# Kernel tuning notes

Measured on AMD Instinct MI355X. Metric: run time of the kernel, lower is better.

The kernel has to match this reference:

```python
import jax, jax.numpy as jnp
import numpy as np

B, S, H, E, V, ML = 64, 256, 512, 256, 32000, 32256  # batch, src len, hidden, embed, vocab, extended vocab


def setup_inputs() -> dict:
    key = jax.random.key(0)
    ks = jax.random.split(key, 14)
    s = 0.02
    return {
        "input_idx": jax.random.randint(ks[0], (B, 1), 0, ML),
        "encoder_outputs": jax.random.normal(ks[1], (B, S, 2 * H), jnp.float32),
        "input_seq_idx": jax.random.randint(ks[2], (B, S), 0, ML),
        "pre_state": jax.random.normal(ks[3], (B, H), jnp.float32),
        "pre_prob_c": jax.random.uniform(ks[4], (B, S), jnp.float32),
        "embed_table": jax.random.normal(ks[5], (V, E), jnp.float32) * s,
        "W_aw": jax.random.normal(ks[6], (2 * H, H), jnp.float32) * s,
        "b_aw": jnp.zeros((2 * H,), jnp.float32),
        "W_ac": jax.random.normal(ks[7], (H, 2 * H + E), jnp.float32) * s,
        "b_ac": jnp.zeros((H,), jnp.float32),
        "W_ih": jax.random.normal(ks[8], (3 * H, 3 * H), jnp.float32) * s,
        "b_ih": jnp.zeros((3 * H,), jnp.float32),
        "W_hh": jax.random.normal(ks[9], (3 * H, H), jnp.float32) * s,
        "b_hh": jnp.zeros((3 * H,), jnp.float32),
        "W_o": jax.random.normal(ks[10], (V, H), jnp.float32) * s,
        "b_o": jnp.zeros((V,), jnp.float32),
        "W_c": jax.random.normal(ks[11], (H, 2 * H), jnp.float32) * s,
        "b_c": jnp.zeros((H,), jnp.float32),
    }


def reference(input_idx, encoder_outputs, input_seq_idx, pre_state, pre_prob_c,
              embed_table, W_aw, b_aw, W_ac, b_ac, W_ih, b_ih, W_hh, b_hh,
              W_o, b_o, W_c, b_c):
    dtype = encoder_outputs.dtype
    Vv = W_o.shape[0]

    # embedding of previous token (OOV -> UNK id 2)
    embed_x = jnp.where(input_idx >= Vv, 2, input_idx)            # [B,1]
    embedding = embed_table[embed_x[:, 0]]                        # [B,E]

    # attentive read
    attn_strength = pre_state @ W_aw.T + b_aw                     # [B,2H]
    attn_scores = jnp.einsum('bsd,bd->bs', encoder_outputs, attn_strength)
    attn_weights = jax.nn.softmax(attn_scores, axis=1)            # [B,S]
    context = jnp.einsum('bs,bsd->bd', attn_weights, encoder_outputs)  # [B,2H]
    attn_reading = jnp.concatenate([context, embedding], axis=1) @ W_ac.T + b_ac  # [B,H]

    # selective read (copy): positions equal to previous output token
    sel_mask = (input_seq_idx == input_idx).astype(dtype)         # [B,S]
    select_weights = sel_mask * pre_prob_c
    select_reading = jnp.einsum('bs,bsd->bd', select_weights, encoder_outputs)  # [B,2H]

    # single GRU step (torch gate order: r, z, n)
    x = jnp.concatenate([attn_reading, select_reading], axis=1)   # [B,3H]
    gi = x @ W_ih.T + b_ih
    gh = pre_state @ W_hh.T + b_hh
    i_r, i_z, i_n = jnp.split(gi, 3, axis=1)
    h_r, h_z, h_n = jnp.split(gh, 3, axis=1)
    r = jax.nn.sigmoid(i_r + h_r)
    z = jax.nn.sigmoid(i_z + h_z)
    n = jnp.tanh(i_n + r * h_n)
    state = (1.0 - z) * n + z * pre_state                         # [B,H]

    # generate + copy scores, joint softmax
    score_g = state @ W_o.T + b_o                                 # [B,V]
    score_c_feat = jnp.tanh(encoder_outputs @ W_c.T + b_c)        # [B,S,H]
    score_c = jnp.einsum('bsh,bh->bs', score_c_feat, state)       # [B,S]
    prob = jax.nn.softmax(jnp.concatenate([score_g, score_c], axis=1), axis=1)
    prob_g, prob_c0 = prob[:, :Vv], prob[:, Vv:]

    # aggregate copy probs over repeated source tokens
    same = (input_seq_idx[:, :, None] == input_seq_idx[:, None, :]).astype(dtype)  # [B,S,S]
    prob_c = jnp.einsum('bi,bij->bj', prob_c0, same)              # [B,S]

    # scatter copy probs into extended vocab (duplicates carry identical values)
    bidx = jnp.arange(prob.shape[0])[:, None]
    out = jnp.zeros((prob.shape[0], ML), dtype).at[bidx, input_seq_idx].set(prob_c, mode='drop')
    out = out + jnp.pad(prob_g, ((0, 0), (0, ML - Vv)))
    return out, state, prob_c
```

## Files before the change

kernel.cpp:

```cpp
#include <hip/hip_runtime.h>
#include <hip/hip_bf16.h>
#include <math.h>

#define BB   64
#define SS   256
#define HH   512
#define HD2  1024
#define EE   256
#define VV   32000
#define MLSZ 32256
#define G3   1536

typedef __attribute__((ext_vector_type(8))) short bhalf8;
typedef __attribute__((ext_vector_type(4))) float f32x4;

__device__ __forceinline__ float wredsum(float v) {
#pragma unroll
  for (int o = 32; o > 0; o >>= 1) v += __shfl_down(v, o);
  return v;
}
__device__ __forceinline__ float wredmax(float v) {
#pragma unroll
  for (int o = 32; o > 0; o >>= 1) v = fmaxf(v, __shfl_down(v, o));
  return v;
}
__device__ __forceinline__ float ftanh(float x) {
  float e = __expf(-2.f * fabsf(x));
  float t = (1.f - e) / (1.f + e);
  return copysignf(t, x);
}
__device__ __forceinline__ float fsigmoid(float x) { return 1.f / (1.f + __expf(-x)); }
__device__ __forceinline__ float dot4(float4 a, float4 b) {
  return a.x*b.x + a.y*b.y + a.z*b.z + a.w*b.w;
}
__device__ __forceinline__ void split2(float x, ushort& h, ushort& l) {
  uint u = __float_as_uint(x);
  uint hr = (u + 0x7fffu + ((u >> 16) & 1u)) & 0xffff0000u;
  h = (ushort)(hr >> 16);
  float r = x - __uint_as_float(hr);
  uint u2 = __float_as_uint(r);
  l = (ushort)((u2 + 0x7fffu + ((u2 >> 16) & 1u)) >> 16);
}

__global__ __launch_bounds__(256) void k_split(
    const float* __restrict__ x, ushort* __restrict__ hi, ushort* __restrict__ lo)
{
  const int i = (blockIdx.x * 256 + threadIdx.x) * 4;
  const float4 v = *(const float4*)&x[i];
  ushort4 h, l;
  split2(v.x, h.x, l.x); split2(v.y, h.y, l.y);
  split2(v.z, h.z, l.z); split2(v.w, h.w, l.w);
  *(ushort4*)&hi[i] = h;
  *(ushort4*)&lo[i] = l;
}

__global__ __launch_bounds__(256) void k_smallgemm(
    const float* __restrict__ A, int lda,
    const float* __restrict__ W, int ldw,
    const float* __restrict__ bias,
    float* __restrict__ C, int ldc, int klen)
{
  __shared__ float As[64][36];
  __shared__ float Ws[64][36];
  const int tid = threadIdx.x;
  const int n0 = blockIdx.x * 64;
  const int kbeg = blockIdx.y * klen;
  const int tb = tid & 15;
  const int tn = tid >> 4;
  float acc[4][4];
#pragma unroll
  for (int i = 0; i < 4; ++i)
#pragma unroll
    for (int j = 0; j < 4; ++j)
      acc[i][j] = (blockIdx.y == 0) ? bias[n0 + tn + 16*j] : 0.f;

  const int rr = tid >> 3;
  const int cc = (tid & 7) * 4;
  for (int kc = kbeg; kc < kbeg + klen; kc += 32) {
    __syncthreads();
#pragma unroll
    for (int r = rr; r < 64; r += 32) {
      *(float4*)&As[r][cc] = *(const float4*)&A[(size_t)r * lda + kc + cc];
      *(float4*)&Ws[r][cc] = *(const float4*)&W[(size_t)(n0 + r) * ldw + kc + cc];
    }
    __syncthreads();
#pragma unroll
    for (int k4 = 0; k4 < 32; k4 += 4) {
      float4 a[4], w[4];
#pragma unroll
      for (int i = 0; i < 4; ++i) a[i] = *(const float4*)&As[tb + 16*i][k4];
#pragma unroll
      for (int j = 0; j < 4; ++j) w[j] = *(const float4*)&Ws[tn + 16*j][k4];
#pragma unroll
      for (int i = 0; i < 4; ++i)
#pragma unroll
        for (int j = 0; j < 4; ++j)
          acc[i][j] += dot4(a[i], w[j]);
    }
  }
#pragma unroll
  for (int i = 0; i < 4; ++i)
#pragma unroll
    for (int j = 0; j < 4; ++j)
      atomicAdd(&C[(size_t)(tb + 16*i) * ldc + n0 + tn + 16*j], acc[i][j]);
}

__global__ __launch_bounds__(256) void k_pass1(
    const float* __restrict__ enc, const float* __restrict__ astr,
    const int* __restrict__ seq, const int* __restrict__ iidx,
    const float* __restrict__ ppc,
    float* __restrict__ scores, float* __restrict__ selread)
{
  const int b  = blockIdx.x >> 2;
  const int sc = blockIdx.x & 3;
  const int tid = threadIdx.x;
  const int lane = tid & 63;
  const int w = tid >> 6;
  __shared__ float sr_s[4][1024];

  const int d0 = lane * 16;
  const float* ap = astr + (size_t)b * HD2 + d0;
  const float4 a0 = *(const float4*)(ap + 0);
  const float4 a1 = *(const float4*)(ap + 4);
  const float4 a2 = *(const float4*)(ap + 8);
  const float4 a3 = *(const float4*)(ap + 12);

  float sr[16];
#pragma unroll
  for (int j = 0; j < 16; ++j) sr[j] = 0.f;

  const int idxb = iidx[b];
  const int sbase = sc * 64 + w * 16;
  for (int si = 0; si < 16; ++si) {
    const int s = sbase + si;
    const float* row = enc + ((size_t)b * SS + s) * HD2 + d0;
    const float4 q0 = *(const float4*)(row + 0);
    const float4 q1 = *(const float4*)(row + 4);
    const float4 q2 = *(const float4*)(row + 8);
    const float4 q3 = *(const float4*)(row + 12);
    float dot = dot4(q0, a0) + dot4(q1, a1) + dot4(q2, a2) + dot4(q3, a3);
    dot = wredsum(dot);
    if (lane == 0) scores[b * SS + s] = dot;
    const float sw = (seq[b * SS + s] == idxb) ? ppc[b * SS + s] : 0.f;
    if (sw != 0.f) {
      sr[0]  += sw * q0.x; sr[1]  += sw * q0.y; sr[2]  += sw * q0.z; sr[3]  += sw * q0.w;
      sr[4]  += sw * q1.x; sr[5]  += sw * q1.y; sr[6]  += sw * q1.z; sr[7]  += sw * q1.w;
      sr[8]  += sw * q2.x; sr[9]  += sw * q2.y; sr[10] += sw * q2.z; sr[11] += sw * q2.w;
      sr[12] += sw * q3.x; sr[13] += sw * q3.y; sr[14] += sw * q3.z; sr[15] += sw * q3.w;
    }
  }
#pragma unroll
  for (int j = 0; j < 16; ++j) sr_s[w][d0 + j] = sr[j];
  __syncthreads();
#pragma unroll
  for (int j = 0; j < 4; ++j) {
    const int d = tid * 4 + j;
    const float v = sr_s[0][d] + sr_s[1][d] + sr_s[2][d] + sr_s[3][d];
    atomicAdd(&selread[(size_t)b * HD2 + d], v);
  }
}

__global__ __launch_bounds__(256) void k_softmax_s(float* __restrict__ scores)
{
  const int b = blockIdx.x;
  const int tid = threadIdx.x;
  const int lane = tid & 63, w = tid >> 6;
  __shared__ float red[4];
  __shared__ float bm, bsum;
  float x = scores[b * SS + tid];
  float m = wredmax(x);
  if (lane == 0) red[w] = m;
  __syncthreads();
  if (tid == 0) bm = fmaxf(fmaxf(red[0], red[1]), fmaxf(red[2], red[3]));
  __syncthreads();
  float e = __expf(x - bm);
  float s = wredsum(e);
  if (lane == 0) red[w] = s;
  __syncthreads();
  if (tid == 0) bsum = red[0] + red[1] + red[2] + red[3];
  __syncthreads();
  scores[b * SS + tid] = e / bsum;
}

__global__ __launch_bounds__(256) void k_pass2(
    const float* __restrict__ enc, const float* __restrict__ wgt,
    float* __restrict__ context)
{
  const int b  = blockIdx.x >> 2;
  const int sc = blockIdx.x & 3;
  const int tid = threadIdx.x;
  const int lane = tid & 63;
  const int w = tid >> 6;
  __shared__ float cs[4][1024];
  const int d0 = lane * 16;
  float a[16];
#pragma unroll
  for (int j = 0; j < 16; ++j) a[j] = 0.f;
  const int sbase = sc * 64 + w * 16;
  for (int si = 0; si < 16; ++si) {
    const int s = sbase + si;
    const float wt = wgt[b * SS + s];
    const float* row = enc + ((size_t)b * SS + s) * HD2 + d0;
    const float4 q0 = *(const float4*)(row + 0);
    const float4 q1 = *(const float4*)(row + 4);
    const float4 q2 = *(const float4*)(row + 8);
    const float4 q3 = *(const float4*)(row + 12);
    a[0]  += wt * q0.x; a[1]  += wt * q0.y; a[2]  += wt * q0.z; a[3]  += wt * q0.w;
    a[4]  += wt * q1.x; a[5]  += wt * q1.y; a[6]  += wt * q1.z; a[7]  += wt * q1.w;
    a[8]  += wt * q2.x; a[9]  += wt * q2.y; a[10] += wt * q2.z; a[11] += wt * q2.w;
    a[12] += wt * q3.x; a[13] += wt * q3.y; a[14] += wt * q3.z; a[15] += wt * q3.w;
  }
#pragma unroll
  for (int j = 0; j < 16; ++j) cs[w][d0 + j] = a[j];
  __syncthreads();
#pragma unroll
  for (int j = 0; j < 4; ++j) {
    const int d = tid * 4 + j;
    atomicAdd(&context[(size_t)b * HD2 + d],
              cs[0][d] + cs[1][d] + cs[2][d] + cs[3][d]);
  }
}

__global__ __launch_bounds__(256) void k_cat1(
    const float* __restrict__ context, const float* __restrict__ embed,
    const int* __restrict__ iidx, const float* __restrict__ selread,
    float* __restrict__ cat1, float* __restrict__ xbuf)
{
  const int b = blockIdx.x;
  const int tid = threadIdx.x;
  for (int d = tid; d < HD2; d += 256) {
    cat1[(size_t)b * 1280 + d] = context[(size_t)b * HD2 + d];
    xbuf[(size_t)b * G3 + 512 + d] = selread[(size_t)b * HD2 + d];
  }
  int ei = iidx[b];
  if (ei >= VV) ei = 2;
  cat1[(size_t)b * 1280 + 1024 + tid] = embed[(size_t)ei * EE + tid];
}

__global__ __launch_bounds__(256) void k_gru(
    const float* __restrict__ gi, const float* __restrict__ gh,
    const float* __restrict__ ps, float* __restrict__ st)
{
  const int t = blockIdx.x * 256 + threadIdx.x;
  const int b = t >> 9, h = t & 511;
  const float* gib = gi + (size_t)b * G3;
  const float* ghb = gh + (size_t)b * G3;
  const float r = fsigmoid(gib[h] + ghb[h]);
  const float z = fsigmoid(gib[512 + h] + ghb[512 + h]);
  const float n = ftanh(gib[1024 + h] + r * ghb[1024 + h]);
  st[t] = (1.f - z) * n + z * ps[t];
}

__global__ __launch_bounds__(256) void k_score_g(
    const float* __restrict__ st, const float* __restrict__ Wo,
    const float* __restrict__ bo, float* __restrict__ sg)
{
  __shared__ float Ss[64][36];
  __shared__ float Ws[128][36];
  const int tid = threadIdx.x;
  const int n0 = blockIdx.x * 128;
  const int tb = tid & 15;
  const int tn = tid >> 4;
  float acc[4][8];
#pragma unroll
  for (int i = 0; i < 4; ++i)
#pragma unroll
    for (int j = 0; j < 8; ++j) acc[i][j] = 0.f;

  const int rr = tid >> 3;
  const int cc = (tid & 7) * 4;
  for (int kc = 0; kc < 512; kc += 32) {
    __syncthreads();
#pragma unroll
    for (int r = rr; r < 64; r += 32)
      *(float4*)&Ss[r][cc] = *(const float4*)&st[(size_t)r * 512 + kc + cc];
#pragma unroll
    for (int r = rr; r < 128; r += 32)
      *(float4*)&Ws[r][cc] = *(const float4*)&Wo[(size_t)(n0 + r) * 512 + kc + cc];
    __syncthreads();
#pragma unroll
    for (int k4 = 0; k4 < 32; k4 += 4) {
      float4 a[4], w[8];
#pragma unroll
      for (int i = 0; i < 4; ++i) a[i] = *(const float4*)&Ss[tb + 16*i][k4];
#pragma unroll
      for (int j = 0; j < 8; ++j) w[j] = *(const float4*)&Ws[tn + 16*j][k4];
#pragma unroll
      for (int i = 0; i < 4; ++i)
#pragma unroll
        for (int j = 0; j < 8; ++j)
          acc[i][j] += dot4(a[i], w[j]);
    }
  }
#pragma unroll
  for (int i = 0; i < 4; ++i)
#pragma unroll
    for (int j = 0; j < 8; ++j)
      sg[(size_t)(tb + 16*i) * VV + n0 + tn + 16*j] = acc[i][j] + bo[n0 + tn + 16*j];
}

__global__ __launch_bounds__(256) void k_score_c(
    const float* __restrict__ enc,
    const ushort* __restrict__ whi, const ushort* __restrict__ wlo,
    const float* __restrict__ bc, const float* __restrict__ st,
    float* __restrict__ scc)
{
  __shared__ ushort sAhi[128 * 32];
  __shared__ ushort sAlo[128 * 32];
  __shared__ ushort sBhi[128 * 32];
  __shared__ ushort sBlo[128 * 32];

  const int tid = threadIdx.x;
  const int m0 = blockIdx.x * 128;
  const int n0 = blockIdx.y * 128;
  const int b  = m0 >> 8;
  const int lane = tid & 63;
  const int wid = tid >> 6;
  const int wr = wid >> 1, wc = wid & 1;
  const int kg = lane >> 4;
  const int rl = lane & 15;

  f32x4 acc[4][4];
#pragma unroll
  for (int m = 0; m < 4; ++m)
#pragma unroll
    for (int n = 0; n < 4; ++n) acc[m][n] = (f32x4){0.f, 0.f, 0.f, 0.f};

  const int ar = tid >> 3;
  const int ak = (tid & 7) * 4;
  const int br = tid >> 2;
  const int bs = tid & 3;

  for (int kc = 0; kc < 1024; kc += 32) {
    __syncthreads();
#pragma unroll
    for (int swp = 0; swp < 4; ++swp) {
      const int row = ar + swp * 32;
      const float4 v = *(const float4*)&enc[(size_t)(m0 + row) * 1024 + kc + ak];
      ushort4 h, l;
      split2(v.x, h.x, l.x); split2(v.y, h.y, l.y);
      split2(v.z, h.z, l.z); split2(v.w, h.w, l.w);
      const int sw = (row + (row >> 2)) & 3;
      const int off = row * 64 + (((ak >> 3) ^ sw) * 16) + (ak & 7) * 2;
      *(ushort4*)((char*)sAhi + off) = h;
      *(ushort4*)((char*)sAlo + off) = l;
    }
#pragma unroll
    for (int swp = 0; swp < 2; ++swp) {
      const int row = br + swp * 64;
      const size_t g = (size_t)(n0 + row) * 1024 + kc + bs * 8;
      const uint4 hv = *(const uint4*)&whi[g];
      const uint4 lv = *(const uint4*)&wlo[g];
      const int sw = (row + (row >> 2)) & 3;
      const int off = row * 64 + ((bs ^ sw) * 16);
      *(uint4*)((char*)sBhi + off) = hv;
      *(uint4*)((char*)sBlo + off) = lv;
    }
    __syncthreads();
    bhalf8 ahi[4], alo[4], bhi[4], blo[4];
#pragma unroll
    for (int m = 0; m < 4; ++m) {
      const int row = wr * 64 + m * 16 + rl;
      const int off = row * 64 + ((kg ^ ((row + (row >> 2)) & 3)) * 16);
      ahi[m] = *(const bhalf8*)((const char*)sAhi + off);
      alo[m] = *(const bhalf8*)((const char*)sAlo + off);
    }
#pragma unroll
    for (int n = 0; n < 4; ++n) {
      const int row = wc * 64 + n * 16 + rl;
      const int off = row * 64 + ((kg ^ ((row + (row >> 2)) & 3)) * 16);
      bhi[n] = *(const bhalf8*)((const char*)sBhi + off);
      blo[n] = *(const bhalf8*)((const char*)sBlo + off);
    }
#pragma unroll
    for (int m = 0; m < 4; ++m)
#pragma unroll
      for (int n = 0; n < 4; ++n) {
        acc[m][n] = __builtin_amdgcn_mfma_f32_16x16x32_bf16(ahi[m], bhi[n], acc[m][n], 0, 0, 0);
        acc[m][n] = __builtin_amdgcn_mfma_f32_16x16x32_bf16(ahi[m], blo[n], acc[m][n], 0, 0, 0);
        acc[m][n] = __builtin_amdgcn_mfma_f32_16x16x32_bf16(alo[m], bhi[n], acc[m][n], 0, 0, 0);
      }
  }

  float bcv[4], stv[4];
#pragma unroll
  for (int n = 0; n < 4; ++n) {
    const int col = n0 + wc * 64 + n * 16 + rl;
    bcv[n] = bc[col];
    stv[n] = st[(size_t)b * 512 + col];
  }
  float rs[4][4];
#pragma unroll
  for (int m = 0; m < 4; ++m)
#pragma unroll
    for (int r = 0; r < 4; ++r) {
      float p = 0.f;
#pragma unroll
      for (int n = 0; n < 4; ++n)
        p += ftanh(acc[m][n][r] + bcv[n]) * stv[n];
      rs[m][r] = p;
    }
#pragma unroll
  for (int off = 1; off < 16; off <<= 1)
#pragma unroll
    for (int m = 0; m < 4; ++m)
#pragma unroll
      for (int r = 0; r < 4; ++r)
        rs[m][r] += __shfl_xor(rs[m][r], off);
  if (rl == 0) {
#pragma unroll
    for (int m = 0; m < 4; ++m)
#pragma unroll
      for (int r = 0; r < 4; ++r) {
        const int srow = (m0 & 255) + wr * 64 + m * 16 + kg * 4 + r;
        atomicAdd(&scc[b * SS + srow], rs[m][r]);
      }
  }
}

__global__ __launch_bounds__(1024) void k_bigsoftmax(
    const float* __restrict__ sg, const float* __restrict__ scc,
    float* __restrict__ out, float* __restrict__ pc0, float* __restrict__ stats)
{
  const int b = blockIdx.x;
  const int tid = threadIdx.x;
  const int lane = tid & 63, w = tid >> 6;
  __shared__ float red[16];
  __shared__ float bm, bsum;
  const float* sgb = sg + (size_t)b * VV;
  const float* scb = scc + (size_t)b * SS;

  float m = -3.0e38f;
  for (int v = tid; v < VV; v += 1024) m = fmaxf(m, sgb[v]);
  if (tid < SS) m = fmaxf(m, scb[tid]);
  m = wredmax(m);
  if (lane == 0) red[w] = m;
  __syncthreads();
  if (tid == 0) {
    float t = red[0];
    for (int i = 1; i < 16; ++i) t = fmaxf(t, red[i]);
    bm = t;
  }
  __syncthreads();
  const float mx = bm;

  float s = 0.f;
  for (int v = tid; v < VV; v += 1024) s += __expf(sgb[v] - mx);
  if (tid < SS) s += __expf(scb[tid] - mx);
  s = wredsum(s);
  if (lane == 0) red[w] = s;
  __syncthreads();
  if (tid == 0) {
    float t = 0.f;
    for (int i = 0; i < 16; ++i) t += red[i];
    bsum = t;
  }
  __syncthreads();
  const float inv = 1.f / bsum;
  if (tid == 0) { stats[2*b] = mx; stats[2*b + 1] = inv; }

  float* outb = out + (size_t)b * MLSZ;
  for (int v = tid; v < VV; v += 1024) outb[v] = __expf(sgb[v] - mx) * inv;
  if (tid < SS) {
    pc0[b * SS + tid] = __expf(scb[tid] - mx) * inv;
    outb[VV + tid] = 0.f;
  }
}

__global__ __launch_bounds__(256) void k_probc(
    const int* __restrict__ seq, const float* __restrict__ pc0,
    float* __restrict__ pcout)
{
  const int b = blockIdx.x;
  const int tid = threadIdx.x;
  __shared__ int sq[256];
  __shared__ float pp[256];
  sq[tid] = seq[b * SS + tid];
  pp[tid] = pc0[b * SS + tid];
  __syncthreads();
  const int mys = sq[tid];
  float acc = 0.f;
  for (int i = 0; i < 256; ++i) acc += (sq[i] == mys) ? pp[i] : 0.f;
  pcout[b * SS + tid] = acc;
}

__global__ __launch_bounds__(256) void k_scatter(
    const int* __restrict__ seq, const float* __restrict__ pcout,
    const float* __restrict__ sg, const float* __restrict__ stats,
    float* __restrict__ out)
{
  const int b = blockIdx.x;
  const int tid = threadIdx.x;
  const int v = seq[b * SS + tid];
  if (v < 0 || v >= MLSZ) return;
  float val = pcout[b * SS + tid];
  if (v < VV) val += __expf(sg[(size_t)b * VV + v] - stats[2*b]) * stats[2*b + 1];
  out[(size_t)b * MLSZ + v] = val;
}

extern "C" void kernel_launch(void* const* d_in, const int* in_sizes, int n_in,
                              void* d_out, int out_size, void* d_ws, size_t ws_size,
                              hipStream_t stream)
{
  (void)in_sizes; (void)n_in; (void)out_size; (void)ws_size;
  const int*   input_idx = (const int*)d_in[0];
  const float* enc       = (const float*)d_in[1];
  const int*   seq       = (const int*)d_in[2];
  const float* pre_state = (const float*)d_in[3];
  const float* ppc       = (const float*)d_in[4];
  const float* embed     = (const float*)d_in[5];
  const float* W_aw = (const float*)d_in[6];  const float* b_aw = (const float*)d_in[7];
  const float* W_ac = (const float*)d_in[8];  const float* b_ac = (const float*)d_in[9];
  const float* W_ih = (const float*)d_in[10]; const float* b_ih = (const float*)d_in[11];
  const float* W_hh = (const float*)d_in[12]; const float* b_hh = (const float*)d_in[13];
  const float* W_o  = (const float*)d_in[14]; const float* b_o  = (const float*)d_in[15];
  const float* W_c  = (const float*)d_in[16]; const float* b_c  = (const float*)d_in[17];

  float* out   = (float*)d_out;
  float* st    = out + (size_t)BB * MLSZ;
  float* pcout = st + BB * HH;

  float* ws      = (float*)d_ws;
  float* astr    = ws;
  float* gh      = astr    + 65536;
  float* xbuf    = gh      + 98304;
  float* gi      = xbuf    + 98304;
  float* selread = gi      + 98304;
  float* context = selread + 65536;
  float* scc     = context + 65536;
  const size_t zlen = 65536 + 98304 + 98304 + 98304 + 65536 + 65536 + 16384;
  float* scores  = scc     + 16384;
  float* cat1    = scores  + 16384;
  float* sg      = cat1    + 81920;
  float* pc0     = sg      + 2048000;
  float* stats   = pc0     + 16384;
  ushort* whi    = (ushort*)(stats + 128);
  ushort* wlo    = whi + 524288;

  hipMemsetAsync(ws, 0, zlen * sizeof(float), stream);

  k_split<<<512, 256, 0, stream>>>(W_c, whi, wlo);

  k_smallgemm<<<dim3(16, 2), 256, 0, stream>>>(pre_state, 512, W_aw, 512, b_aw, astr, 1024, 256);
  k_smallgemm<<<dim3(24, 2), 256, 0, stream>>>(pre_state, 512, W_hh, 512, b_hh, gh, 1536, 256);
  k_pass1<<<256, 256, 0, stream>>>(enc, astr, seq, input_idx, ppc, scores, selread);
  k_softmax_s<<<64, 256, 0, stream>>>(scores);
  k_pass2<<<256, 256, 0, stream>>>(enc, scores, context);
  k_cat1<<<64, 256, 0, stream>>>(context, embed, input_idx, selread, cat1, xbuf);
  k_smallgemm<<<dim3(8, 2), 256, 0, stream>>>(cat1, 1280, W_ac, 1280, b_ac, xbuf, 1536, 640);
  k_smallgemm<<<dim3(24, 4), 256, 0, stream>>>(xbuf, 1536, W_ih, 1536, b_ih, gi, 1536, 384);
  k_gru<<<128, 256, 0, stream>>>(gi, gh, pre_state, st);
  k_score_g<<<250, 256, 0, stream>>>(st, W_o, b_o, sg);
  k_score_c<<<dim3(128, 4), 256, 0, stream>>>(enc, whi, wlo, b_c, st, scc);
  k_bigsoftmax<<<64, 1024, 0, stream>>>(sg, scc, out, pc0, stats);
  k_probc<<<64, 256, 0, stream>>>(seq, pc0, pcout);
  k_scatter<<<64, 256, 0, stream>>>(seq, pcout, sg, stats, out);
}
```

Before: 542.8 us.

## Use bf16 MFMA for score_g and pre-permute W_c fragments for score_c

The FP32 SIMT GEMM for the generate scores (state @ W_o^T) becomes single-pass bf16 MFMA. The state is first rounded to bf16 and permuted into fragment order, and W_o is converted to bf16 in registers. W_c is split into hi/lo bf16 halves that are stored in MFMA fragment order, so score_c can load B fragments straight from global memory. That lets score_c drop its B shared-memory staging and move to 512-thread blocks covering all 512 columns, which removes the duplicated encoder loads across the old column blocks. The catch is that score_g now runs at plain bf16 precision instead of fp32, so the generate logits lose accuracy.

```diff
diff --git a/kernel.cpp b/kernel.cpp
--- a/kernel.cpp
+++ b/kernel.cpp
@@ -33,6 +33,10 @@
 __device__ __forceinline__ float dot4(float4 a, float4 b) {
   return a.x*b.x + a.y*b.y + a.z*b.z + a.w*b.w;
 }
+__device__ __forceinline__ ushort bf16rne(float x) {
+  uint u = __float_as_uint(x);
+  return (ushort)((u + 0x7fffu + ((u >> 16) & 1u)) >> 16);
+}
 __device__ __forceinline__ void split2(float x, ushort& h, ushort& l) {
   uint u = __float_as_uint(x);
   uint hr = (u + 0x7fffu + ((u >> 16) & 1u)) & 0xffff0000u;
@@ -42,16 +46,43 @@
   l = (ushort)((u2 + 0x7fffu + ((u2 >> 16) & 1u)) >> 16);
 }
 
-__global__ __launch_bounds__(256) void k_split(
-    const float* __restrict__ x, ushort* __restrict__ hi, ushort* __restrict__ lo)
-{
-  const int i = (blockIdx.x * 256 + threadIdx.x) * 4;
-  const float4 v = *(const float4*)&x[i];
-  ushort4 h, l;
-  split2(v.x, h.x, l.x); split2(v.y, h.y, l.y);
-  split2(v.z, h.z, l.z); split2(v.w, h.w, l.w);
-  *(ushort4*)&hi[i] = h;
-  *(ushort4*)&lo[i] = l;
+__global__ __launch_bounds__(256) void k_split_wc(
+    const float* __restrict__ Wc, ushort* __restrict__ bhi, ushort* __restrict__ blo)
+{
+  const int tid = blockIdx.x * 256 + threadIdx.x;
+  const int col = tid >> 7;
+  const int g   = tid & 127;
+  const float* p = Wc + (size_t)col * 1024 + g * 8;
+  const float4 v0 = *(const float4*)p;
+  const float4 v1 = *(const float4*)(p + 4);
+  ushort h[8], l[8];
+  split2(v0.x, h[0], l[0]); split2(v0.y, h[1], l[1]);
+  split2(v0.z, h[2], l[2]); split2(v0.w, h[3], l[3]);
+  split2(v1.x, h[4], l[4]); split2(v1.y, h[5], l[5]);
+  split2(v1.z, h[6], l[6]); split2(v1.w, h[7], l[7]);
+  const int lane = ((g & 3) << 4) | (col & 15);
+  const int kc = g >> 2, nf = col >> 4;
+  const size_t dst = (((size_t)(nf * 32 + kc)) * 64 + lane) * 8;
+  *(ushort4*)&bhi[dst] = make_ushort4(h[0], h[1], h[2], h[3]);
+  *(ushort4*)&bhi[dst + 4] = make_ushort4(h[4], h[5], h[6], h[7]);
+  *(ushort4*)&blo[dst] = make_ushort4(l[0], l[1], l[2], l[3]);
+  *(ushort4*)&blo[dst + 4] = make_ushort4(l[4], l[5], l[6], l[7]);
+}
+
+__global__ __launch_bounds__(256) void k_split_state(
+    const float* __restrict__ st, ushort* __restrict__ ap)
+{
+  const int tid = blockIdx.x * 256 + threadIdx.x;
+  const int row = tid >> 6;
+  const int g   = tid & 63;
+  const float* p = st + (size_t)row * 512 + g * 8;
+  const float4 v0 = *(const float4*)p;
+  const float4 v1 = *(const float4*)(p + 4);
+  const int lane = ((g & 3) << 4) | (row & 15);
+  const int kc = g >> 2, mf = row >> 4;
+  const size_t dst = (((size_t)(mf * 16 + kc)) * 64 + lane) * 8;
+  *(ushort4*)&ap[dst] = make_ushort4(bf16rne(v0.x), bf16rne(v0.y), bf16rne(v0.z), bf16rne(v0.w));
+  *(ushort4*)&ap[dst + 4] = make_ushort4(bf16rne(v1.x), bf16rne(v1.y), bf16rne(v1.z), bf16rne(v1.w));
 }
 
 __global__ __launch_bounds__(256) void k_smallgemm(
@@ -252,73 +283,64 @@
 }
 
 __global__ __launch_bounds__(256) void k_score_g(
-    const float* __restrict__ st, const float* __restrict__ Wo,
+    const ushort* __restrict__ ap, const float* __restrict__ Wo,
     const float* __restrict__ bo, float* __restrict__ sg)
 {
-  __shared__ float Ss[64][36];
-  __shared__ float Ws[128][36];
-  const int tid = threadIdx.x;
-  const int n0 = blockIdx.x * 128;
-  const int tb = tid & 15;
-  const int tn = tid >> 4;
-  float acc[4][8];
-#pragma unroll
-  for (int i = 0; i < 4; ++i)
-#pragma unroll
-    for (int j = 0; j < 8; ++j) acc[i][j] = 0.f;
-
-  const int rr = tid >> 3;
-  const int cc = (tid & 7) * 4;
-  for (int kc = 0; kc < 512; kc += 32) {
-    __syncthreads();
-#pragma unroll
-    for (int r = rr; r < 64; r += 32)
-      *(float4*)&Ss[r][cc] = *(const float4*)&st[(size_t)r * 512 + kc + cc];
-#pragma unroll
-    for (int r = rr; r < 128; r += 32)
-      *(float4*)&Ws[r][cc] = *(const float4*)&Wo[(size_t)(n0 + r) * 512 + kc + cc];
-    __syncthreads();
-#pragma unroll
-    for (int k4 = 0; k4 < 32; k4 += 4) {
-      float4 a[4], w[8];
-#pragma unroll
-      for (int i = 0; i < 4; ++i) a[i] = *(const float4*)&Ss[tb + 16*i][k4];
-#pragma unroll
-      for (int j = 0; j < 8; ++j) w[j] = *(const float4*)&Ws[tn + 16*j][k4];
-#pragma unroll
-      for (int i = 0; i < 4; ++i)
-#pragma unroll
-        for (int j = 0; j < 8; ++j)
-          acc[i][j] += dot4(a[i], w[j]);
-    }
-  }
-#pragma unroll
-  for (int i = 0; i < 4; ++i)
-#pragma unroll
-    for (int j = 0; j < 8; ++j)
-      sg[(size_t)(tb + 16*i) * VV + n0 + tn + 16*j] = acc[i][j] + bo[n0 + tn + 16*j];
-}
-
-__global__ __launch_bounds__(256) void k_score_c(
+  const int tid = threadIdx.x;
+  const int lane = tid & 63;
+  const int wid = tid >> 6;
+  const int rl = lane & 15, kg = lane >> 4;
+  const int n0 = blockIdx.x * 64;
+  const int col = n0 + wid * 16 + rl;
+  const float* wrow = Wo + (size_t)col * 512 + kg * 8;
+
+  f32x4 acc[4];
+#pragma unroll
+  for (int m = 0; m < 4; ++m) acc[m] = (f32x4){0.f, 0.f, 0.f, 0.f};
+
+#pragma unroll 4
+  for (int kc = 0; kc < 16; ++kc) {
+    const float4 w0 = *(const float4*)(wrow + kc * 32);
+    const float4 w1 = *(const float4*)(wrow + kc * 32 + 4);
+    bhalf8 bh;
+    bh[0] = (short)bf16rne(w0.x); bh[1] = (short)bf16rne(w0.y);
+    bh[2] = (short)bf16rne(w0.z); bh[3] = (short)bf16rne(w0.w);
+    bh[4] = (short)bf16rne(w1.x); bh[5] = (short)bf16rne(w1.y);
+    bh[6] = (short)bf16rne(w1.z); bh[7] = (short)bf16rne(w1.w);
+#pragma unroll
+    for (int m = 0; m < 4; ++m) {
+      const bhalf8 a = *(const bhalf8*)(ap + (((size_t)(m * 16 + kc)) * 64 + lane) * 8);
+      acc[m] = __builtin_amdgcn_mfma_f32_16x16x32_bf16(a, bh, acc[m], 0, 0, 0);
+    }
+  }
+  const float bv = bo[col];
+#pragma unroll
+  for (int m = 0; m < 4; ++m)
+#pragma unroll
+    for (int r = 0; r < 4; ++r)
+      sg[(size_t)(m * 16 + kg * 4 + r) * VV + col] = acc[m][r] + bv;
+}
+
+__global__ __launch_bounds__(512) void k_score_c(
     const float* __restrict__ enc,
-    const ushort* __restrict__ whi, const ushort* __restrict__ wlo,
+    const ushort* __restrict__ wfh, const ushort* __restrict__ wfl,
     const float* __restrict__ bc, const float* __restrict__ st,
     float* __restrict__ scc)
 {
-  __shared__ ushort sAhi[128 * 32];
-  __shared__ ushort sAlo[128 * 32];
-  __shared__ ushort sBhi[128 * 32];
-  __shared__ ushort sBlo[128 * 32];
-
-  const int tid = threadIdx.x;
-  const int m0 = blockIdx.x * 128;
-  const int n0 = blockIdx.y * 128;
-  const int b  = m0 >> 8;
+  __shared__ ushort sAhi[64 * 32];
+  __shared__ ushort sAlo[64 * 32];
+  const int tid = threadIdx.x;
   const int lane = tid & 63;
   const int wid = tid >> 6;
-  const int wr = wid >> 1, wc = wid & 1;
-  const int kg = lane >> 4;
-  const int rl = lane & 15;
+  const int rl = lane & 15, kg = lane >> 4;
+  const int m0 = blockIdx.x * 64;
+  const int b = m0 >> 8;
+
+  const int srow = tid >> 3;
+  const int skq = (tid & 7) * 4;
+  const int ssw = (srow + (srow >> 2)) & 3;
+  const int soff = srow * 64 + (((skq >> 3) ^ ssw) * 16) + (skq & 7) * 2;
+  const float* aseg = enc + (size_t)(m0 + srow) * 1024 + skq;
 
   f32x4 acc[4][4];
 #pragma unroll
@@ -326,51 +348,29 @@
 #pragma unroll
     for (int n = 0; n < 4; ++n) acc[m][n] = (f32x4){0.f, 0.f, 0.f, 0.f};
 
-  const int ar = tid >> 3;
-  const int ak = (tid & 7) * 4;
-  const int br = tid >> 2;
-  const int bs = tid & 3;
-
-  for (int kc = 0; kc < 1024; kc += 32) {
+  for (int kc = 0; kc < 32; ++kc) {
     __syncthreads();
-#pragma unroll
-    for (int swp = 0; swp < 4; ++swp) {
-      const int row = ar + swp * 32;
-      const float4 v = *(const float4*)&enc[(size_t)(m0 + row) * 1024 + kc + ak];
-      ushort4 h, l;
-      split2(v.x, h.x, l.x); split2(v.y, h.y, l.y);
-      split2(v.z, h.z, l.z); split2(v.w, h.w, l.w);
-      const int sw = (row + (row >> 2)) & 3;
-      const int off = row * 64 + (((ak >> 3) ^ sw) * 16) + (ak & 7) * 2;
-      *(ushort4*)((char*)sAhi + off) = h;
-      *(ushort4*)((char*)sAlo + off) = l;
-    }
-#pragma unroll
-    for (int swp = 0; swp < 2; ++swp) {
-      const int row = br + swp * 64;
-      const size_t g = (size_t)(n0 + row) * 1024 + kc + bs * 8;
-      const uint4 hv = *(const uint4*)&whi[g];
-      const uint4 lv = *(const uint4*)&wlo[g];
-      const int sw = (row + (row >> 2)) & 3;
-      const int off = row * 64 + ((bs ^ sw) * 16);
-      *(uint4*)((char*)sBhi + off) = hv;
-      *(uint4*)((char*)sBlo + off) = lv;
+    const float4 v = *(const float4*)(aseg + kc * 32);
+    ushort4 h, l;
+    split2(v.x, h.x, l.x); split2(v.y, h.y, l.y);
+    split2(v.z, h.z, l.z); split2(v.w, h.w, l.w);
+    *(ushort4*)((char*)sAhi + soff) = h;
+    *(ushort4*)((char*)sAlo + soff) = l;
+    bhalf8 bhi[4], blo[4];
+#pragma unroll
+    for (int n = 0; n < 4; ++n) {
+      const size_t src = (((size_t)((wid * 4 + n) * 32 + kc)) * 64 + lane) * 8;
+      bhi[n] = *(const bhalf8*)(wfh + src);
+      blo[n] = *(const bhalf8*)(wfl + src);
     }
     __syncthreads();
-    bhalf8 ahi[4], alo[4], bhi[4], blo[4];
+    bhalf8 ahi[4], alo[4];
 #pragma unroll
     for (int m = 0; m < 4; ++m) {
-      const int row = wr * 64 + m * 16 + rl;
+      const int row = m * 16 + rl;
       const int off = row * 64 + ((kg ^ ((row + (row >> 2)) & 3)) * 16);
       ahi[m] = *(const bhalf8*)((const char*)sAhi + off);
       alo[m] = *(const bhalf8*)((const char*)sAlo + off);
-    }
-#pragma unroll
-    for (int n = 0; n < 4; ++n) {
-      const int row = wc * 64 + n * 16 + rl;
-      const int off = row * 64 + ((kg ^ ((row + (row >> 2)) & 3)) * 16);
-      bhi[n] = *(const bhalf8*)((const char*)sBhi + off);
-      blo[n] = *(const bhalf8*)((const char*)sBlo + off);
     }
 #pragma unroll
     for (int m = 0; m < 4; ++m)
@@ -385,9 +385,9 @@
   float bcv[4], stv[4];
 #pragma unroll
   for (int n = 0; n < 4; ++n) {
-    const int col = n0 + wc * 64 + n * 16 + rl;
-    bcv[n] = bc[col];
-    stv[n] = st[(size_t)b * 512 + col];
+    const int c = (wid * 4 + n) * 16 + rl;
+    bcv[n] = bc[c];
+    stv[n] = st[(size_t)b * 512 + c];
   }
   float rs[4][4];
 #pragma unroll
@@ -411,10 +411,8 @@
 #pragma unroll
     for (int m = 0; m < 4; ++m)
 #pragma unroll
-      for (int r = 0; r < 4; ++r) {
-        const int srow = (m0 & 255) + wr * 64 + m * 16 + kg * 4 + r;
-        atomicAdd(&scc[b * SS + srow], rs[m][r]);
-      }
+      for (int r = 0; r < 4; ++r)
+        atomicAdd(&scc[b * SS + (m0 & 255) + m * 16 + kg * 4 + r], rs[m][r]);
   }
 }
 
@@ -534,12 +532,13 @@
   float* sg      = cat1    + 81920;
   float* pc0     = sg      + 2048000;
   float* stats   = pc0     + 16384;
-  ushort* whi    = (ushort*)(stats + 128);
-  ushort* wlo    = whi + 524288;
+  ushort* wfh    = (ushort*)(stats + 128);
+  ushort* wfl    = wfh + 524288;
+  ushort* stperm = wfl + 524288;
 
   hipMemsetAsync(ws, 0, zlen * sizeof(float), stream);
 
-  k_split<<<512, 256, 0, stream>>>(W_c, whi, wlo);
+  k_split_wc<<<256, 256, 0, stream>>>(W_c, wfh, wfl);
 
   k_smallgemm<<<dim3(16, 2), 256, 0, stream>>>(pre_state, 512, W_aw, 512, b_aw, astr, 1024, 256);
   k_smallgemm<<<dim3(24, 2), 256, 0, stream>>>(pre_state, 512, W_hh, 512, b_hh, gh, 1536, 256);
@@ -550,8 +549,9 @@
   k_smallgemm<<<dim3(8, 2), 256, 0, stream>>>(cat1, 1280, W_ac, 1280, b_ac, xbuf, 1536, 640);
   k_smallgemm<<<dim3(24, 4), 256, 0, stream>>>(xbuf, 1536, W_ih, 1536, b_ih, gi, 1536, 384);
   k_gru<<<128, 256, 0, stream>>>(gi, gh, pre_state, st);
-  k_score_g<<<250, 256, 0, stream>>>(st, W_o, b_o, sg);
-  k_score_c<<<dim3(128, 4), 256, 0, stream>>>(enc, whi, wlo, b_c, st, scc);
+  k_split_state<<<16, 256, 0, stream>>>(st, stperm);
+  k_score_g<<<500, 256, 0, stream>>>(stperm, W_o, b_o, sg);
+  k_score_c<<<256, 512, 0, stream>>>(enc, wfh, wfl, b_c, st, scc);
   k_bigsoftmax<<<64, 1024, 0, stream>>>(sg, scc, out, pc0, stats);
   k_probc<<<64, 256, 0, stream>>>(seq, pc0, pcout);
   k_scatter<<<64, 256, 0, stream>>>(seq, pcout, sg, stats, out);
```

New measurement: 479.0 us. 1.13x faster.
